# Kernel optimization log

Hardware: AMD Instinct MI355X
Metric: run time of the kernel (lower is better)

## Reference

```python
import jax, jax.numpy as jnp
import numpy as np

NC = 80
T0, T1 = 0.0025, 0.0225  # scale_area_thresholds
BOX_W, OBJ_W, CLS_W = 5.0, 1.0, 1.0
BOOST = 2.0  # small_object_boost


def setup_inputs() -> dict:
    key = jax.random.key(0)
    ks = jax.random.split(key, 9)
    B, A, T = 16, 3, 100
    grids = [(80, 80), (40, 40), (20, 20)]
    outs = [jax.random.normal(ks[i], (B, A, h, w, 5 + NC), jnp.float32)
            for i, (h, w) in enumerate(grids)]
    # targets: [B, T, 5] = (x1, y1, x2, y2, class_id) in normalized coords
    cx = jax.random.uniform(ks[3], (B, T), minval=0.05, maxval=0.95)
    cy = jax.random.uniform(ks[4], (B, T), minval=0.05, maxval=0.95)
    # log-uniform sides -> areas span both thresholds (all 3 scales hit)
    bw = 10.0 ** jax.random.uniform(ks[5], (B, T), minval=-2.3, maxval=-0.6)
    bh = 10.0 ** jax.random.uniform(ks[6], (B, T), minval=-2.3, maxval=-0.6)
    cls_id = jnp.floor(jax.random.uniform(ks[7], (B, T)) * NC)
    targets = jnp.stack([cx - bw / 2, cy - bh / 2, cx + bw / 2, cy + bh / 2, cls_id], axis=-1).astype(jnp.float32)
    return {"out0": outs[0], "out1": outs[1], "out2": outs[2], "targets": targets}


def _bce(logits, t):
    # BCEWithLogits: log(1+e^x) - x*t, numerically stable via logaddexp
    return jnp.logaddexp(0.0, logits) - logits * t


def _iou_xyxy(b1, b2, eps=1e-6):
    x1 = jnp.maximum(b1[..., 0], b2[..., 0]); y1 = jnp.maximum(b1[..., 1], b2[..., 1])
    x2 = jnp.minimum(b1[..., 2], b2[..., 2]); y2 = jnp.minimum(b1[..., 3], b2[..., 3])
    inter = jnp.clip(x2 - x1, 0.0) * jnp.clip(y2 - y1, 0.0)
    a1 = jnp.clip(b1[..., 2] - b1[..., 0], 0.0) * jnp.clip(b1[..., 3] - b1[..., 1], 0.0)
    a2 = jnp.clip(b2[..., 2] - b2[..., 0], 0.0) * jnp.clip(b2[..., 3] - b2[..., 1], 0.0)
    return inter / (a1 + a2 - inter + eps)


def _build_targets(tgts, scale_index, A, H, W):
    """Sequential (order-faithful) scatter of GT boxes onto the grid; vmapped over batch."""
    def per_image(tg):  # tg: [T, 5]
        init = (jnp.zeros((H, W), jnp.float32), jnp.zeros((H, W, 4), jnp.float32),
                jnp.zeros((H, W, NC), jnp.float32), jnp.ones((H, W), jnp.float32))

        def step(carry, t):
            obj, box, cls, w = carry
            x1 = jnp.clip(t[0], 0.0, 1.0); y1 = jnp.clip(t[1], 0.0, 1.0)
            x2 = jnp.clip(t[2], 0.0, 1.0); y2 = jnp.clip(t[3], 0.0, 1.0)
            valid = (x2 > x1) & (y2 > y1)
            area = (x2 - x1) * (y2 - y1)
            sidx = jnp.where(area <= T0, 0, jnp.where(area <= T1, 1, 2))
            valid = valid & (sidx == scale_index)
            gi = jnp.clip(jnp.floor(0.5 * (x1 + x2) * W).astype(jnp.int32), 0, W - 1)
            gj = jnp.clip(jnp.floor(0.5 * (y1 + y2) * H).astype(jnp.int32), 0, H - 1)
            cid = t[4].astype(jnp.int32)
            cls_ok = (cid >= 0) & (cid < NC)
            cidc = jnp.clip(cid, 0, NC - 1)
            smallness = 1.0 - jnp.minimum(1.0, area / max(T0, 1e-6))
            weight = 1.0 + (BOOST - 1.0) * jnp.maximum(0.0, smallness)
            bvec = jnp.stack([x1, y1, x2, y2])
            obj = obj.at[gj, gi].set(jnp.where(valid, 1.0, obj[gj, gi]))
            box = box.at[gj, gi].set(jnp.where(valid, bvec, box[gj, gi]))
            cls = cls.at[gj, gi, cidc].set(jnp.where(valid & cls_ok, 1.0, cls[gj, gi, cidc]))
            w = w.at[gj, gi].set(jnp.where(valid, weight, w[gj, gi]))
            tiny = valid & (area <= T0)
            for dj, di in ((-1, 0), (1, 0), (0, -1), (0, 1)):
                nj, ni = gj + dj, gi + di
                ok = tiny & (nj >= 0) & (nj < H) & (ni >= 0) & (ni < W)
                njc = jnp.clip(nj, 0, H - 1); nic = jnp.clip(ni, 0, W - 1)
                obj = obj.at[njc, nic].set(jnp.where(ok, jnp.maximum(obj[njc, nic], 0.5), obj[njc, nic]))
                box = box.at[njc, nic].set(jnp.where(ok, bvec, box[njc, nic]))
                cls = cls.at[njc, nic, cidc].set(jnp.where(ok & cls_ok, 1.0, cls[njc, nic, cidc]))
                w = w.at[njc, nic].set(jnp.where(ok, jnp.maximum(w[njc, nic], 0.5 * weight), w[njc, nic]))
            return (obj, box, cls, w), None

        (obj, box, cls, w), _ = jax.lax.scan(step, init, tg)
        return obj, box, cls, w

    obj, box, cls, w = jax.vmap(per_image)(tgts)
    B = tgts.shape[0]
    # only anchor 0 is ever assigned (anchor_id = 0 in the original)
    obj_f = jnp.zeros((B, A, H, W), jnp.float32).at[:, 0].set(obj)
    box_f = jnp.zeros((B, A, H, W, 4), jnp.float32).at[:, 0].set(box)
    cls_f = jnp.zeros((B, A, H, W, NC), jnp.float32).at[:, 0].set(cls)
    w_f = jnp.ones((B, A, H, W), jnp.float32).at[:, 0].set(w)
    return obj_f, box_f, cls_f, w_f


def _scale_loss(out, tgts, scale_index):
    B, A, H, W, _ = out.shape
    reg, objp, clsp = out[..., :4], out[..., 4], out[..., 5:]
    obj_t, box_t, cls_t, sw = _build_targets(tgts, scale_index, A, H, W)
    obj_loss = _bce(objp, obj_t).mean()
    pos = obj_t > 0.5
    npos = jnp.sum(pos)
    denom = jnp.maximum(npos, 1).astype(jnp.float32)
    pb = jax.nn.sigmoid(reg)
    d = pb - box_t
    ad = jnp.abs(d)
    l1 = jnp.where(ad < 1.0, 0.5 * d * d, ad - 0.5).mean(-1)  # smooth_l1, beta=1
    box_per = (l1 + 1.0 - _iou_xyxy(pb, box_t)) * sw
    box_loss = jnp.where(npos > 0, jnp.sum(jnp.where(pos, box_per, 0.0)) / denom, 0.0)
    cls_per = _bce(clsp, cls_t).mean(-1) * sw
    cls_loss = jnp.where(npos > 0, jnp.sum(jnp.where(pos, cls_per, 0.0)) / denom, 0.0)
    return box_loss, obj_loss, cls_loss


def reference(out0, out1, out2, targets):
    targets = jax.lax.stop_gradient(targets)  # torch builds targets from python floats (detached)
    outs = (out0, out1, out2)
    bl = ol = cl = 0.0
    for s, o in enumerate(outs):
        b, ob, c = _scale_loss(o, targets, s)
        bl, ol, cl = bl + b, ol + ob, cl + c
    n = float(len(outs))
    bl, ol, cl = bl / n, ol / n, cl / n
    final = BOX_W * bl + OBJ_W * ol + CLS_W * cl
    return final, bl, ol, cl
```

## Files before the change

### kernel.cpp

```cpp
#include <hip/hip_runtime.h>
#include <math.h>

#define NCLS 80
#define NB 16
#define NA 3
#define NT 100

static constexpr int TOTCELLS  = 134400;
static constexpr int CELL_OFF1 = 102400;
static constexpr int CELL_OFF2 = 128000;

static constexpr int OBJ_TOT  = 403200;
static constexpr int OBJ_OFF1 = 307200;
static constexpr int OBJ_OFF2 = 384000;

__device__ unsigned g_lastMain[TOTCELLS];
__device__ unsigned g_lastAny [TOTCELLS];
__device__ unsigned g_maskA   [TOTCELLS*3];
__device__ float4   g_bvec  [NB*NT];
__device__ float    g_weight[NB*NT];
__device__ double   g_objsum[3];
__device__ double   g_boxsum[3];
__device__ double   g_clssum[3];
__device__ unsigned g_npos  [3];
__device__ unsigned g_posCount;
__device__ unsigned g_posList[NB*NT];

__device__ __forceinline__ float softplusf(float x) {
    return fmaxf(x, 0.0f) + log1pf(expf(-fabsf(x)));
}

__global__ __launch_bounds__(256) void k_clear() {
    int i = blockIdx.x * 256 + threadIdx.x;
    g_lastMain[i] = 0u;
    g_lastAny[i]  = 0u;
    g_maskA[3*i+0] = 0u; g_maskA[3*i+1] = 0u; g_maskA[3*i+2] = 0u;
    if (i < 3) { g_objsum[i] = 0.0; g_boxsum[i] = 0.0; g_clssum[i] = 0.0; g_npos[i] = 0u; }
    if (i == 0) g_posCount = 0u;
}

__global__ __launch_bounds__(256) void k_scatter(const float* __restrict__ tgt) {
    int idx = blockIdx.x * 256 + threadIdx.x;
    if (idx >= NB * NT) return;
    int b = idx / NT, t = idx % NT;
    const float* p = tgt + (size_t)idx * 5;
    float x1 = fminf(fmaxf(p[0], 0.0f), 1.0f);
    float y1 = fminf(fmaxf(p[1], 0.0f), 1.0f);
    float x2 = fminf(fmaxf(p[2], 0.0f), 1.0f);
    float y2 = fminf(fmaxf(p[3], 0.0f), 1.0f);
    bool valid = (x2 > x1) && (y2 > y1);
    float area = (x2 - x1) * (y2 - y1);
    int sidx = (area <= 0.0025f) ? 0 : ((area <= 0.0225f) ? 1 : 2);
    int Wd = (sidx == 0) ? 80 : ((sidx == 1) ? 40 : 20);
    int HWc = Wd * Wd;
    int soff = (sidx == 0) ? 0 : ((sidx == 1) ? CELL_OFF1 : CELL_OFF2);

    int gi = (int)floorf(0.5f * (x1 + x2) * (float)Wd);
    int gj = (int)floorf(0.5f * (y1 + y2) * (float)Wd);
    gi = min(max(gi, 0), Wd - 1);
    gj = min(max(gj, 0), Wd - 1);

    int cid = (int)p[4];
    bool cls_ok = (cid >= 0) && (cid < NCLS);
    float smallness = 1.0f - fminf(1.0f, area / 0.0025f);
    float weight = 1.0f + fmaxf(0.0f, smallness);

    g_bvec[idx]   = make_float4(x1, y1, x2, y2);
    g_weight[idx] = weight;

    if (!valid) return;
    unsigned seq = (unsigned)(t + 1);
    int cell = soff + b * HWc + gj * Wd + gi;
    atomicMax(&g_lastMain[cell], seq);
    atomicMax(&g_lastAny[cell],  seq);
    if (cls_ok) atomicOr(&g_maskA[3*cell + (cid >> 5)], 1u << (cid & 31));

    if (area <= 0.0025f) {
        const int dj[4] = {-1, 1, 0, 0};
        const int di[4] = {0, 0, -1, 1};
        #pragma unroll
        for (int k = 0; k < 4; ++k) {
            int nj = gj + dj[k], ni = gi + di[k];
            if (nj >= 0 && nj < Wd && ni >= 0 && ni < Wd) {
                int nc = soff + b * HWc + nj * Wd + ni;
                atomicMax(&g_lastAny[nc], seq);
                if (cls_ok) atomicOr(&g_maskA[3*nc + (cid >> 5)], 1u << (cid & 31));
            }
        }
    }
}

__global__ __launch_bounds__(256) void k_obj(const float* __restrict__ o0,
                                             const float* __restrict__ o1,
                                             const float* __restrict__ o2) {
    __shared__ double sred[256];
    int n = blockIdx.x * 256 + threadIdx.x;
    int s, loc, HW, soff;
    const float* out;
    if (n < OBJ_OFF1)      { s = 0; loc = n;            out = o0; HW = 6400; soff = 0; }
    else if (n < OBJ_OFF2) { s = 1; loc = n - OBJ_OFF1; out = o1; HW = 1600; soff = CELL_OFF1; }
    else                   { s = 2; loc = n - OBJ_OFF2; out = o2; HW = 400;  soff = CELL_OFF2; }
    int b = loc / (NA * HW);
    int r = loc % (NA * HW);
    int a = r / HW;
    int cij = r % HW;

    float x = out[(size_t)loc * 85 + 4];
    float contrib = softplusf(x);
    if (a == 0) {
        int cell = soff + b * HW + cij;
        unsigned lm = g_lastMain[cell];
        float tv = lm ? 1.0f : (g_lastAny[cell] ? 0.5f : 0.0f);
        contrib -= x * tv;
        if (lm) {
            unsigned slot = atomicAdd(&g_posCount, 1u);
            g_posList[slot] = (unsigned)cell;
            atomicAdd(&g_npos[s], 1u);
        }
    }
    sred[threadIdx.x] = (double)contrib;
    __syncthreads();
    for (int st = 128; st > 0; st >>= 1) {
        if (threadIdx.x < st) sred[threadIdx.x] += sred[threadIdx.x + st];
        __syncthreads();
    }
    if (threadIdx.x == 0) atomicAdd(&g_objsum[s], sred[0]);
}

__global__ __launch_bounds__(256) void k_poswork(const float* __restrict__ o0,
                                                 const float* __restrict__ o1,
                                                 const float* __restrict__ o2) {
    __shared__ double sB[4], sC[4];
    __shared__ int    sS[4];
    int wv   = threadIdx.x >> 6;
    int lane = threadIdx.x & 63;
    int w = blockIdx.x * 4 + wv;
    unsigned count = g_posCount;

    double bsum = 0.0, csum = 0.0;
    int sidx = -1;
    if (w < (int)count) {
        int n = (int)g_posList[w];
        int s, b, cij, HW;
        const float* out;
        if (n < CELL_OFF1)      { s = 0; HW = 6400; int l = n;             b = l / 6400; cij = l % 6400; out = o0; }
        else if (n < CELL_OFF2) { s = 1; HW = 1600; int l = n - CELL_OFF1; b = l / 1600; cij = l % 1600; out = o1; }
        else                    { s = 2; HW = 400;  int l = n - CELL_OFF2; b = l / 400;  cij = l % 400;  out = o2; }
        sidx = s;

        const float* base = out + ((size_t)(b * NA * HW) + (size_t)cij) * 85;
        float v0 = base[lane];
        float v1 = (lane < 21) ? base[64 + lane] : 0.0f;

        unsigned m0 = g_maskA[3*n], m1 = g_maskA[3*n+1], m2 = g_maskA[3*n+2];
        unsigned lm = g_lastMain[n], la = g_lastAny[n];
        float4 bt = g_bvec[b * NT + (int)(la - 1u)];
        float  sw = g_weight[b * NT + (int)(lm - 1u)];

        float cl_ = 0.0f;
        if (lane >= 5) {
            int c = lane - 5;
            unsigned bit = ((c < 32) ? (m0 >> c) : (m1 >> (c - 32))) & 1u;
            cl_ += softplusf(v0) - (bit ? v0 : 0.0f);
        }
        if (lane < 21) {
            int c = lane + 59;
            unsigned bit = ((c < 64) ? (m1 >> (c - 32)) : (m2 >> (c - 64))) & 1u;
            cl_ += softplusf(v1) - (bit ? v1 : 0.0f);
        }

        float pv = 1.0f / (1.0f + expf(-v0));
        float pb0 = __shfl(pv, 0), pb1 = __shfl(pv, 1), pb2 = __shfl(pv, 2), pb3 = __shfl(pv, 3);

        #pragma unroll
        for (int off = 32; off > 0; off >>= 1) cl_ += __shfl_xor(cl_, off);

        if (lane == 0) {
            float btv[4] = {bt.x, bt.y, bt.z, bt.w};
            float pb[4]  = {pb0, pb1, pb2, pb3};
            float l1 = 0.0f;
            #pragma unroll
            for (int k = 0; k < 4; ++k) {
                float d = pb[k] - btv[k];
                float ad = fabsf(d);
                l1 += (ad < 1.0f) ? (0.5f * d * d) : (ad - 0.5f);
            }
            l1 *= 0.25f;
            float ix1 = fmaxf(pb0, bt.x), iy1 = fmaxf(pb1, bt.y);
            float ix2 = fminf(pb2, bt.z), iy2 = fminf(pb3, bt.w);
            float inter = fmaxf(ix2 - ix1, 0.0f) * fmaxf(iy2 - iy1, 0.0f);
            float a1 = fmaxf(pb2 - pb0, 0.0f) * fmaxf(pb3 - pb1, 0.0f);
            float a2 = fmaxf(bt.z - bt.x, 0.0f) * fmaxf(bt.w - bt.y, 0.0f);
            float iou = inter / (a1 + a2 - inter + 1e-6f);
            bsum = (double)((l1 + 1.0f - iou) * sw);
            csum = (double)(cl_ * (1.0f / (float)NCLS) * sw);
        }
    }

    if (lane == 0) { sB[wv] = bsum; sC[wv] = csum; sS[wv] = sidx; }
    __syncthreads();
    if (threadIdx.x == 0) {
        double accB[3] = {0.0, 0.0, 0.0};
        double accC[3] = {0.0, 0.0, 0.0};
        #pragma unroll
        for (int i = 0; i < 4; ++i) {
            int si = sS[i];
            if (si >= 0) { accB[si] += sB[i]; accC[si] += sC[i]; }
        }
        #pragma unroll
        for (int s2 = 0; s2 < 3; ++s2) {
            if (accB[s2] != 0.0) atomicAdd(&g_boxsum[s2], accB[s2]);
            if (accC[s2] != 0.0) atomicAdd(&g_clssum[s2], accC[s2]);
        }
    }
}

__global__ void k_final(float* __restrict__ d_out) {
    if (threadIdx.x != 0 || blockIdx.x != 0) return;
    const double cells[3] = {307200.0, 76800.0, 19200.0};
    double bl = 0.0, ol = 0.0, cl = 0.0;
    for (int s = 0; s < 3; ++s) {
        ol += g_objsum[s] / cells[s];
        unsigned np = g_npos[s];
        if (np > 0u) {
            double denom = (double)np;
            bl += g_boxsum[s] / denom;
            cl += g_clssum[s] / denom;
        }
    }
    bl /= 3.0; ol /= 3.0; cl /= 3.0;
    double fin = 5.0 * bl + 1.0 * ol + 1.0 * cl;
    d_out[0] = (float)fin;
    d_out[1] = (float)bl;
    d_out[2] = (float)ol;
    d_out[3] = (float)cl;
}

extern "C" void kernel_launch(void* const* d_in, const int* in_sizes, int n_in,
                              void* d_out, int out_size, void* d_ws, size_t ws_size,
                              hipStream_t stream) {
    const float* o0 = (const float*)d_in[0];
    const float* o1 = (const float*)d_in[1];
    const float* o2 = (const float*)d_in[2];
    const float* tg = (const float*)d_in[3];
    float* outp = (float*)d_out;

    k_clear   <<<TOTCELLS / 256, 256, 0, stream>>>();
    k_scatter <<<(NB * NT + 255) / 256, 256, 0, stream>>>(tg);
    k_obj     <<<OBJ_TOT / 256, 256, 0, stream>>>(o0, o1, o2);
    k_poswork <<<(NB * NT + 3) / 4, 256, 0, stream>>>(o0, o1, o2);
    k_final   <<<1, 64, 0, stream>>>(outp);
}
```

Measured before the change: 75.21 us.

## Decouple objectness softplus pass from target scatter and fuse final reduction

Folds the workspace clear into the big objectness pass, which now computes only the target-independent softplus sum and writes per-block partials instead of doing double atomics. The target-dependent -x*t term becomes a per-target correction computed in a small kernel that checks the winner and neighbour cells. The final reduction moves into the poswork kernel through a last-block-done counter, which drops one launch. The cost is more complex correctness logic (seq matching, threadfence and atomic reads) and a strided partial sum in the poswork blocks.

```diff
diff --git a/kernel.cpp b/kernel.cpp
--- a/kernel.cpp
+++ b/kernel.cpp
@@ -13,30 +13,60 @@
 static constexpr int OBJ_TOT  = 403200;
 static constexpr int OBJ_OFF1 = 307200;
 static constexpr int OBJ_OFF2 = 384000;
+
+static constexpr int K1_BLOCKS = OBJ_TOT / 256;
+static constexpr int K4_BLOCKS = 400;
 
 __device__ unsigned g_lastMain[TOTCELLS];
 __device__ unsigned g_lastAny [TOTCELLS];
 __device__ unsigned g_maskA   [TOTCELLS*3];
 __device__ float4   g_bvec  [NB*NT];
 __device__ float    g_weight[NB*NT];
+__device__ double   g_partial[K1_BLOCKS];
 __device__ double   g_objsum[3];
+__device__ double   g_objcorr[3];
 __device__ double   g_boxsum[3];
 __device__ double   g_clssum[3];
 __device__ unsigned g_npos  [3];
 __device__ unsigned g_posCount;
 __device__ unsigned g_posList[NB*NT];
+__device__ unsigned g_done;
 
 __device__ __forceinline__ float softplusf(float x) {
     return fmaxf(x, 0.0f) + log1pf(expf(-fabsf(x)));
 }
 
-__global__ __launch_bounds__(256) void k_clear() {
-    int i = blockIdx.x * 256 + threadIdx.x;
-    g_lastMain[i] = 0u;
-    g_lastAny[i]  = 0u;
-    g_maskA[3*i+0] = 0u; g_maskA[3*i+1] = 0u; g_maskA[3*i+2] = 0u;
-    if (i < 3) { g_objsum[i] = 0.0; g_boxsum[i] = 0.0; g_clssum[i] = 0.0; g_npos[i] = 0u; }
-    if (i == 0) g_posCount = 0u;
+__device__ __forceinline__ double wred64(double v) {
+    #pragma unroll
+    for (int o = 32; o > 0; o >>= 1) v += __shfl_xor(v, o);
+    return v;
+}
+
+__global__ __launch_bounds__(256) void k1_clear_obj(const float* __restrict__ o0,
+                                                    const float* __restrict__ o1,
+                                                    const float* __restrict__ o2) {
+    __shared__ double sw4[4];
+    int n = blockIdx.x * 256 + threadIdx.x;
+    g_maskA[n] = 0u;
+    if (n < TOTCELLS) { g_lastMain[n] = 0u; g_lastAny[n] = 0u; }
+    if (n == 0) {
+        #pragma unroll
+        for (int s = 0; s < 3; ++s) {
+            g_objsum[s] = 0.0; g_objcorr[s] = 0.0;
+            g_boxsum[s] = 0.0; g_clssum[s] = 0.0;
+            g_npos[s] = 0u;
+        }
+        g_posCount = 0u; g_done = 0u;
+    }
+    const float* out; int loc;
+    if (n < OBJ_OFF1)      { out = o0; loc = n; }
+    else if (n < OBJ_OFF2) { out = o1; loc = n - OBJ_OFF1; }
+    else                   { out = o2; loc = n - OBJ_OFF2; }
+    float x = out[(size_t)loc * 85 + 4];
+    double v = wred64((double)softplusf(x));
+    if ((threadIdx.x & 63) == 0) sw4[threadIdx.x >> 6] = v;
+    __syncthreads();
+    if (threadIdx.x == 0) g_partial[blockIdx.x] = sw4[0] + sw4[1] + sw4[2] + sw4[3];
 }
 
 __global__ __launch_bounds__(256) void k_scatter(const float* __restrict__ tgt) {
@@ -90,46 +120,77 @@
     }
 }
 
-__global__ __launch_bounds__(256) void k_obj(const float* __restrict__ o0,
-                                             const float* __restrict__ o1,
-                                             const float* __restrict__ o2) {
-    __shared__ double sred[256];
-    int n = blockIdx.x * 256 + threadIdx.x;
-    int s, loc, HW, soff;
-    const float* out;
-    if (n < OBJ_OFF1)      { s = 0; loc = n;            out = o0; HW = 6400; soff = 0; }
-    else if (n < OBJ_OFF2) { s = 1; loc = n - OBJ_OFF1; out = o1; HW = 1600; soff = CELL_OFF1; }
-    else                   { s = 2; loc = n - OBJ_OFF2; out = o2; HW = 400;  soff = CELL_OFF2; }
-    int b = loc / (NA * HW);
-    int r = loc % (NA * HW);
-    int a = r / HW;
-    int cij = r % HW;
-
-    float x = out[(size_t)loc * 85 + 4];
-    float contrib = softplusf(x);
-    if (a == 0) {
-        int cell = soff + b * HW + cij;
-        unsigned lm = g_lastMain[cell];
-        float tv = lm ? 1.0f : (g_lastAny[cell] ? 0.5f : 0.0f);
-        contrib -= x * tv;
-        if (lm) {
-            unsigned slot = atomicAdd(&g_posCount, 1u);
-            g_posList[slot] = (unsigned)cell;
-            atomicAdd(&g_npos[s], 1u);
-        }
-    }
-    sred[threadIdx.x] = (double)contrib;
+__global__ __launch_bounds__(256) void k3_winner(const float* __restrict__ o0,
+                                                 const float* __restrict__ o1,
+                                                 const float* __restrict__ o2,
+                                                 const float* __restrict__ tgt) {
+    __shared__ double sw4[3][4];
+    int idx = blockIdx.x * 256 + threadIdx.x;
+    double corr[3] = {0.0, 0.0, 0.0};
+    if (idx < NB * NT) {
+        int b = idx / NT, t = idx % NT;
+        const float* p = tgt + (size_t)idx * 5;
+        float x1 = fminf(fmaxf(p[0], 0.0f), 1.0f);
+        float y1 = fminf(fmaxf(p[1], 0.0f), 1.0f);
+        float x2 = fminf(fmaxf(p[2], 0.0f), 1.0f);
+        float y2 = fminf(fmaxf(p[3], 0.0f), 1.0f);
+        bool valid = (x2 > x1) && (y2 > y1);
+        if (valid) {
+            float area = (x2 - x1) * (y2 - y1);
+            int sidx = (area <= 0.0025f) ? 0 : ((area <= 0.0225f) ? 1 : 2);
+            int Wd = (sidx == 0) ? 80 : ((sidx == 1) ? 40 : 20);
+            int HWc = Wd * Wd;
+            int soff = (sidx == 0) ? 0 : ((sidx == 1) ? CELL_OFF1 : CELL_OFF2);
+            const float* out = (sidx == 0) ? o0 : ((sidx == 1) ? o1 : o2);
+            int gi = (int)floorf(0.5f * (x1 + x2) * (float)Wd);
+            int gj = (int)floorf(0.5f * (y1 + y2) * (float)Wd);
+            gi = min(max(gi, 0), Wd - 1);
+            gj = min(max(gj, 0), Wd - 1);
+            unsigned seq = (unsigned)(t + 1);
+            int cell = soff + b * HWc + gj * Wd + gi;
+            if (g_lastMain[cell] == seq) {
+                unsigned slot = atomicAdd(&g_posCount, 1u);
+                g_posList[slot] = (unsigned)cell;
+                atomicAdd(&g_npos[sidx], 1u);
+                float x = out[((size_t)(b * NA * HWc) + (size_t)(gj * Wd + gi)) * 85 + 4];
+                corr[sidx] -= (double)x;
+            }
+            if (area <= 0.0025f) {
+                const int dj[4] = {-1, 1, 0, 0};
+                const int di[4] = {0, 0, -1, 1};
+                #pragma unroll
+                for (int k = 0; k < 4; ++k) {
+                    int nj = gj + dj[k], ni = gi + di[k];
+                    if (nj >= 0 && nj < Wd && ni >= 0 && ni < Wd) {
+                        int nc = soff + b * HWc + nj * Wd + ni;
+                        if (g_lastMain[nc] == 0u && g_lastAny[nc] == seq) {
+                            float x = out[((size_t)(b * NA * HWc) + (size_t)(nj * Wd + ni)) * 85 + 4];
+                            corr[sidx] -= 0.5 * (double)x;
+                        }
+                    }
+                }
+            }
+        }
+    }
+    #pragma unroll
+    for (int s = 0; s < 3; ++s) {
+        double r = wred64(corr[s]);
+        if ((threadIdx.x & 63) == 0) sw4[s][threadIdx.x >> 6] = r;
+    }
     __syncthreads();
-    for (int st = 128; st > 0; st >>= 1) {
-        if (threadIdx.x < st) sred[threadIdx.x] += sred[threadIdx.x + st];
-        __syncthreads();
-    }
-    if (threadIdx.x == 0) atomicAdd(&g_objsum[s], sred[0]);
-}
-
-__global__ __launch_bounds__(256) void k_poswork(const float* __restrict__ o0,
-                                                 const float* __restrict__ o1,
-                                                 const float* __restrict__ o2) {
+    if (threadIdx.x == 0) {
+        #pragma unroll
+        for (int s = 0; s < 3; ++s) {
+            double r = sw4[s][0] + sw4[s][1] + sw4[s][2] + sw4[s][3];
+            if (r != 0.0) atomicAdd(&g_objcorr[s], r);
+        }
+    }
+}
+
+__global__ __launch_bounds__(256) void k4_poswork(const float* __restrict__ o0,
+                                                  const float* __restrict__ o1,
+                                                  const float* __restrict__ o2,
+                                                  float* __restrict__ d_out) {
     __shared__ double sB[4], sC[4];
     __shared__ int    sS[4];
     int wv   = threadIdx.x >> 6;
@@ -212,28 +273,38 @@
             if (accB[s2] != 0.0) atomicAdd(&g_boxsum[s2], accB[s2]);
             if (accC[s2] != 0.0) atomicAdd(&g_clssum[s2], accC[s2]);
         }
-    }
-}
-
-__global__ void k_final(float* __restrict__ d_out) {
-    if (threadIdx.x != 0 || blockIdx.x != 0) return;
-    const double cells[3] = {307200.0, 76800.0, 19200.0};
-    double bl = 0.0, ol = 0.0, cl = 0.0;
-    for (int s = 0; s < 3; ++s) {
-        ol += g_objsum[s] / cells[s];
-        unsigned np = g_npos[s];
-        if (np > 0u) {
-            double denom = (double)np;
-            bl += g_boxsum[s] / denom;
-            cl += g_clssum[s] / denom;
-        }
-    }
-    bl /= 3.0; ol /= 3.0; cl /= 3.0;
-    double fin = 5.0 * bl + 1.0 * ol + 1.0 * cl;
-    d_out[0] = (float)fin;
-    d_out[1] = (float)bl;
-    d_out[2] = (float)ol;
-    d_out[3] = (float)cl;
+        double accP[3] = {0.0, 0.0, 0.0};
+        for (int k = blockIdx.x; k < K1_BLOCKS; k += K4_BLOCKS) {
+            int s2 = (k < 1200) ? 0 : ((k < 1500) ? 1 : 2);
+            accP[s2] += g_partial[k];
+        }
+        #pragma unroll
+        for (int s2 = 0; s2 < 3; ++s2)
+            if (accP[s2] != 0.0) atomicAdd(&g_objsum[s2], accP[s2]);
+
+        __threadfence();
+        unsigned old = atomicAdd(&g_done, 1u);
+        if (old == (unsigned)(gridDim.x - 1)) {
+            const double cells[3] = {307200.0, 76800.0, 19200.0};
+            double bl = 0.0, ol = 0.0, cl = 0.0;
+            for (int s = 0; s < 3; ++s) {
+                double os = atomicAdd(&g_objsum[s], 0.0) + atomicAdd(&g_objcorr[s], 0.0);
+                ol += os / cells[s];
+                unsigned np = atomicAdd(&g_npos[s], 0u);
+                if (np > 0u) {
+                    double denom = (double)np;
+                    bl += atomicAdd(&g_boxsum[s], 0.0) / denom;
+                    cl += atomicAdd(&g_clssum[s], 0.0) / denom;
+                }
+            }
+            bl /= 3.0; ol /= 3.0; cl /= 3.0;
+            double fin = 5.0 * bl + 1.0 * ol + 1.0 * cl;
+            d_out[0] = (float)fin;
+            d_out[1] = (float)bl;
+            d_out[2] = (float)ol;
+            d_out[3] = (float)cl;
+        }
+    }
 }
 
 extern "C" void kernel_launch(void* const* d_in, const int* in_sizes, int n_in,
@@ -245,9 +316,8 @@
     const float* tg = (const float*)d_in[3];
     float* outp = (float*)d_out;
 
-    k_clear   <<<TOTCELLS / 256, 256, 0, stream>>>();
-    k_scatter <<<(NB * NT + 255) / 256, 256, 0, stream>>>(tg);
-    k_obj     <<<OBJ_TOT / 256, 256, 0, stream>>>(o0, o1, o2);
-    k_poswork <<<(NB * NT + 3) / 4, 256, 0, stream>>>(o0, o1, o2);
-    k_final   <<<1, 64, 0, stream>>>(outp);
-}
+    k1_clear_obj<<<K1_BLOCKS, 256, 0, stream>>>(o0, o1, o2);
+    k_scatter   <<<(NB * NT + 255) / 256, 256, 0, stream>>>(tg);
+    k3_winner   <<<(NB * NT + 255) / 256, 256, 0, stream>>>(o0, o1, o2, tg);
+    k4_poswork  <<<K4_BLOCKS, 256, 0, stream>>>(o0, o1, o2, outp);
+}
```

Result: faster. 62.36 us (-17.1%).
